# Optimization experiments

Hardware: AMD Instinct MI355X
Metric: run time of the kernel (lower is better)

Reference implementation:

```python
import jax, jax.numpy as jnp
import numpy as np

B, T, D, H, L = 16384, 100, 5, 32, 1  # batch, seq_len, input/output dim, hidden, latent


def setup_inputs() -> dict:
    key = jax.random.key(0)
    ks = jax.random.split(key, 28)
    rn = lambda k, shp, s=0.1: jax.random.normal(k, shp, dtype=jnp.float32) * s
    return {
        "x": rn(ks[0], (B, T, D), 1.0),
        "eps": rn(ks[1], (B, L), 1.0),
        # Encoder LSTM (PyTorch layout: W_ih [4H, D], W_hh [4H, H], gate order i,f,g,o)
        "enc_Wih": rn(ks[2], (4 * H, D)), "enc_Whh": rn(ks[3], (4 * H, H)),
        "enc_bih": rn(ks[4], (4 * H,)), "enc_bhh": rn(ks[5], (4 * H,)),
        "W_mu": rn(ks[6], (L, 2 * H)), "b_mu": rn(ks[7], (L,)),
        "W_lv": rn(ks[8], (L, 2 * H)), "b_lv": rn(ks[9], (L,)),
        # Decoder
        "W_l2h": rn(ks[10], (H, L)), "b_l2h": rn(ks[11], (H,)),
        "W_l2h2": rn(ks[12], (H, L)), "b_l2h2": rn(ks[13], (H,)),
        "start_token": jnp.zeros((1, D), jnp.float32),
        "W_emb": rn(ks[14], (H, D)), "b_emb": rn(ks[15], (H,)),
        "dec_Wih": rn(ks[16], (4 * H, H)), "dec_Whh": rn(ks[17], (4 * H, H)),
        "dec_bih": rn(ks[18], (4 * H,)), "dec_bhh": rn(ks[19], (4 * H,)),
        "W_out": rn(ks[20], (D, H)), "b_out": rn(ks[21], (D,)),
        "W_seq": rn(ks[22], (H, L)), "b_seq": rn(ks[23], (H,)),
        "W_seq2": rn(ks[24], (1, H)), "b_seq2": rn(ks[25], (1,)),
    }


def _lstm_cell(x_t, h, c, Wih, Whh, b):
    g = x_t @ Wih.T + h @ Whh.T + b            # [B, 4H]
    i, f, gg, o = jnp.split(g, 4, axis=-1)      # PyTorch gate order i,f,g,o
    c = jax.nn.sigmoid(f) * c + jax.nn.sigmoid(i) * jnp.tanh(gg)
    h = jax.nn.sigmoid(o) * jnp.tanh(c)
    return h, c


def reference(x, eps, enc_Wih, enc_Whh, enc_bih, enc_bhh, W_mu, b_mu, W_lv, b_lv,
              W_l2h, b_l2h, W_l2h2, b_l2h2, start_token, W_emb, b_emb,
              dec_Wih, dec_Whh, dec_bih, dec_bhh, W_out, b_out,
              W_seq, b_seq, W_seq2, b_seq2):
    bsz, seq_len, _ = x.shape
    hdim = enc_Whh.shape[1]
    lrelu = lambda v: jax.nn.leaky_relu(v, negative_slope=0.01)

    # ---- Encoder LSTM over time ----
    b_enc = enc_bih + enc_bhh
    def enc_step(carry, x_t):
        h, c = carry
        h, c = _lstm_cell(x_t, h, c, enc_Wih, enc_Whh, b_enc)
        return (h, c), None
    z0 = jnp.zeros((bsz, hdim), x.dtype)
    (h_n, c_n), _ = jax.lax.scan(enc_step, (z0, z0), jnp.swapaxes(x, 0, 1))
    hcat = jnp.concatenate([h_n, c_n], axis=-1)        # [B, 2H]
    mu = hcat @ W_mu.T + b_mu                           # [B, L]
    log_var = hcat @ W_lv.T + b_lv                      # [B, L]

    # ---- Reparameterize ----
    z = mu + eps * jnp.exp(0.5 * log_var)

    h0 = lrelu(mu @ W_l2h.T + b_l2h)                    # [B, H]
    c0 = lrelu(mu @ W_l2h2.T + b_l2h2)                  # [B, H]
    x0 = jnp.broadcast_to(start_token @ W_emb.T + b_emb, (bsz, hdim))
    b_dec = dec_bih + dec_bhh
    def dec_step(carry, _):
        x_in, h, c = carry
        x_t = jax.nn.relu(x_in)
        h, c = _lstm_cell(x_t, h, c, dec_Wih, dec_Whh, b_dec)
        return (h, h, c), h
    _, hs = jax.lax.scan(dec_step, (x0, h0, c0), None, length=seq_len)  # [T, B, H]
    recon = jnp.swapaxes(hs, 0, 1) @ W_out.T + b_out    # [B, T, D]

    # ---- num head on z (encoder_outputs arg) ----
    num = jax.nn.relu(lrelu(z @ W_seq.T + b_seq) @ W_seq2.T + b_seq2)  # [B, 1]

    return recon, mu, log_var, num
```

## Files before the change

### kernel.cpp

```cpp
#include <hip/hip_runtime.h>
#include <hip/hip_bf16.h>

typedef short bf16x8 __attribute__((ext_vector_type(8)));
typedef float f32x4  __attribute__((ext_vector_type(4)));
typedef unsigned int u32x4 __attribute__((ext_vector_type(4)));

#define LOG2E 1.44269504088896340736f

static __device__ __forceinline__ unsigned short f2bf(float f){
    __hip_bfloat16 h = __float2bfloat16(f);
    return __builtin_bit_cast(unsigned short, h);
}
static __device__ __forceinline__ float bf2f(unsigned short u){
    unsigned v = ((unsigned)u) << 16;
    return __builtin_bit_cast(float, v);
}
static __device__ __forceinline__ unsigned pk_bf16(float lo, float hi){
    return (((unsigned)f2bf(hi)) << 16) | (unsigned)f2bf(lo);
}
static __device__ __forceinline__ float rcp_(float x){ return __builtin_amdgcn_rcpf(x); }
static __device__ __forceinline__ float ex2(float x){ return __builtin_amdgcn_exp2f(x); }
static __device__ __forceinline__ void lds_fence(){
    asm volatile("s_waitcnt lgkmcnt(0)" ::: "memory");
}
static __device__ __forceinline__ f32x4 mfma16(bf16x8 a, bf16x8 b, f32x4 c){
    return __builtin_amdgcn_mfma_f32_16x16x32_bf16(a, b, c, 0, 0, 0);
}

__global__ void marker_kernel(float* out, int n, float v){
    int i = blockIdx.x * 256 + threadIdx.x;
    if (i < n) out[i] = v;
}

__global__ __launch_bounds__(256, 1)
void vae_mfma3_kernel(const float* __restrict__ x,      const float* __restrict__ eps,
                      const float* __restrict__ eWih,   const float* __restrict__ eWhh,
                      const float* __restrict__ ebih,   const float* __restrict__ ebhh,
                      const float* __restrict__ Wmu,    const float* __restrict__ bmu,
                      const float* __restrict__ Wlv,    const float* __restrict__ blv,
                      const float* __restrict__ Wl2h,   const float* __restrict__ bl2h,
                      const float* __restrict__ Wl2h2,  const float* __restrict__ bl2h2,
                      const float* __restrict__ stok,   const float* __restrict__ Wemb,
                      const float* __restrict__ bemb,
                      const float* __restrict__ dWih,   const float* __restrict__ dWhh,
                      const float* __restrict__ dbih,   const float* __restrict__ dbhh,
                      const float* __restrict__ Wout,   const float* __restrict__ bout,
                      const float* __restrict__ Wseq,   const float* __restrict__ bseq,
                      const float* __restrict__ Wseq2,  const float* __restrict__ bseq2,
                      float* __restrict__ recon,
                      float* __restrict__ out_mu,
                      float* __restrict__ out_lv,
                      float* __restrict__ out_num)
{
    __shared__ float hbf[4][16][33];
    __shared__ float cbf[4][16][33];
    __shared__ float mubuf[4][16];
    __shared__ float x0buf[4][32];
    __shared__ float cw[524];

    const int tid = threadIdx.x;
    const int w   = tid >> 6;
    const int l   = tid & 63;
    const int c   = l & 15;
    const int g   = l >> 4;
    const int bbase = blockIdx.x * 64 + w * 16;

    if (tid < 64){ cw[tid] = Wmu[tid]; cw[64+tid] = Wlv[tid]; }
    if (tid < 32){
        cw[128+tid] = Wseq[tid];  cw[160+tid] = bseq[tid];  cw[192+tid] = Wseq2[tid];
        cw[224+tid] = Wl2h[tid];  cw[256+tid] = bl2h[tid];
        cw[288+tid] = Wl2h2[tid]; cw[320+tid] = bl2h2[tid];
    }
    if (tid < 160) cw[352+tid] = Wout[tid];
    if (tid < 5)   cw[512+tid] = bout[tid];
    if (tid == 0){ cw[517] = bmu[0]; cw[518] = blv[0]; cw[519] = bseq2[0]; }
    __syncthreads();

    bf16x8 WH[8], WX[8];
    f32x4  biasv[8];
    #pragma unroll
    for (int n=0;n<8;++n){
        const int gt = n>>1, half = n&1;
        const float sc = (gt==2) ? (-2.0f*LOG2E) : (-LOG2E);
        const int GRc = gt*32 + ((c>>2)<<3) + half*4 + (c&3);
        bf16x8 t;
        #pragma unroll
        for (int j=0;j<8;++j) t[j] = (short)f2bf(sc * eWhh[(size_t)GRc*32 + g*8 + j]);
        WH[n] = t;
        bf16x8 tx = (bf16x8)0;
        if (g == 0){
            #pragma unroll
            for (int j=0;j<5;++j) tx[j] = (short)f2bf(sc * eWih[(size_t)GRc*5 + j]);
        }
        WX[n] = tx;
        f32x4 b4;
        #pragma unroll
        for (int q=0;q<4;++q){
            const int R = gt*32 + g*8 + half*4 + q;
            b4[q] = sc * (ebih[R] + ebhh[R]);
        }
        biasv[n] = b4;
    }

    float cs[8], hn[8];
    #pragma unroll
    for (int k=0;k<8;++k){ cs[k] = 0.0f; hn[k] = 0.0f; }
    u32x4 hpk = (u32x4)0;

    float4 xA = {0,0,0,0}; float xB = 0.0f;
    if (g == 0){
        const float* xp = x + (size_t)(bbase+c)*500;
        xA = *(const float4*)xp; xB = xp[4];
    }

    for (int t=0; t<100; ++t){
        bf16x8 bx = (bf16x8)0;
        if (g == 0){
            bx[0]=(short)f2bf(xA.x); bx[1]=(short)f2bf(xA.y);
            bx[2]=(short)f2bf(xA.z); bx[3]=(short)f2bf(xA.w);
            bx[4]=(short)f2bf(xB);
            if (t < 99){
                const float* xp = x + (size_t)(bbase+c)*500 + (t+1)*5;
                xA = *(const float4*)xp; xB = xp[4];
            }
        }
        bf16x8 bh = __builtin_bit_cast(bf16x8, hpk);

        f32x4 acc[8];
        #pragma unroll
        for (int n=0;n<8;++n){
            f32x4 a = mfma16(WX[n], bx, biasv[n]);
            acc[n] = mfma16(WH[n], bh, a);
        }

        #pragma unroll
        for (int q=0;q<4;++q){
          #pragma unroll
          for (int u=0;u<2;++u){
            const int ul = u*4 + q;
            float ei = ex2(acc[0+u][q]);
            float ef = ex2(acc[2+u][q]);
            float eg = ex2(acc[4+u][q]);
            float eo = ex2(acc[6+u][q]);
            float pig = (1.0f+ei)*(1.0f+eg);
            float num = cs[ul]*pig + (1.0f+ef)*(1.0f-eg);
            float cn  = num * rcp_((1.0f+ef)*pig);
            float ec  = ex2(cn * (-2.0f*LOG2E));
            hn[ul]    = (1.0f-ec) * rcp_((1.0f+eo)*(1.0f+ec));
            cs[ul]    = cn;
          }
        }
        hpk[0] = pk_bf16(hn[0], hn[1]);
        hpk[1] = pk_bf16(hn[2], hn[3]);
        hpk[2] = pk_bf16(hn[4], hn[5]);
        hpk[3] = pk_bf16(hn[6], hn[7]);
    }

    #pragma unroll
    for (int ul=0; ul<8; ++ul){
        hbf[w][c][g*8+ul] = hn[ul];
        cbf[w][c][g*8+ul] = cs[ul];
    }
    lds_fence();

    bf16x8 WI[8], WHd[8];
    f32x4  dbias[8];
    #pragma unroll
    for (int n=0;n<8;++n){
        const int gt = n>>1, half = n&1;
        const float sc = (gt==2) ? (-2.0f*LOG2E) : (-LOG2E);
        const int GRc = gt*32 + ((c>>2)<<3) + half*4 + (c&3);
        bf16x8 ti, th;
        #pragma unroll
        for (int j=0;j<8;++j){
            ti[j] = (short)f2bf(sc * dWih[(size_t)GRc*32 + g*8 + j]);
            th[j] = (short)f2bf(sc * dWhh[(size_t)GRc*32 + g*8 + j]);
        }
        WI[n] = ti; WHd[n] = th;
        f32x4 b4;
        #pragma unroll
        for (int q=0;q<4;++q){
            const int R = gt*32 + g*8 + half*4 + q;
            b4[q] = sc * (dbih[R] + dbhh[R]);
        }
        dbias[n] = b4;
    }
    bf16x8 WO = (bf16x8)0;
    f32x4 bosv = (f32x4)0;
    if (c < 5){
        bf16x8 to;
        #pragma unroll
        for (int j=0;j<8;++j) to[j] = (short)f2bf(Wout[c*32 + g*8 + j]);
        WO = to;
    }
    #pragma unroll
    for (int q=0;q<4;++q){
        const int dd = g*4 + q;
        bosv[q] = (dd < 5) ? bout[dd] : 0.0f;
    }

    if (l < 16){
        const int r = l;
        float mu = cw[517], lv = cw[518];
        #pragma unroll
        for (int k=0;k<32;++k){
            float hvv = hbf[w][r][k], cvv = cbf[w][r][k];
            mu += hvv*cw[k]    + cvv*cw[32+k];
            lv += hvv*cw[64+k] + cvv*cw[96+k];
        }
        out_mu[bbase+r] = mu;
        out_lv[bbase+r] = lv;
        mubuf[w][r] = mu;
        float z = mu + eps[bbase+r] * __builtin_amdgcn_exp2f(0.5f*LOG2E*lv);
        float a2 = cw[519];
        #pragma unroll
        for (int j=0;j<32;++j){
            float s = z*cw[128+j] + cw[160+j];
            s = s > 0.0f ? s : 0.01f*s;
            a2 += cw[192+j]*s;
        }
        out_num[bbase+r] = fmaxf(a2, 0.0f);
    }
    if (l < 32){
        float v = bemb[l];
        #pragma unroll
        for (int d=0; d<5; ++d) v += stok[d]*Wemb[l*5 + d];
        x0buf[w][l] = fmaxf(v, 0.0f);
    }
    lds_fence();

    {
        const float muv = mubuf[w][c];
        #pragma unroll
        for (int ul=0; ul<8; ++ul){
            const int U = g*8 + ul;
            float a = muv*cw[224+U] + cw[256+U];
            float b = muv*cw[288+U] + cw[320+U];
            hn[ul] = (a > 0.0f ? a : 0.01f*a);
            cs[ul] = (b > 0.0f ? b : 0.01f*b);
        }
        hpk[0] = pk_bf16(hn[0], hn[1]);
        hpk[1] = pk_bf16(hn[2], hn[3]);
        hpk[2] = pk_bf16(hn[4], hn[5]);
        hpk[3] = pk_bf16(hn[6], hn[7]);
    }
    bf16x8 bx0;
    #pragma unroll
    for (int j=0;j<8;++j) bx0[j] = (short)f2bf(x0buf[w][g*8 + j]);

    for (int t=0; t<100; ++t){
        bf16x8 bh = __builtin_bit_cast(bf16x8, hpk);

        if (t > 0){
            f32x4 ao = mfma16(WO, bh, bosv);
            float* rp = recon + (size_t)(bbase+c)*500 + (t-1)*5;
            if (g == 0){ rp[0]=ao[0]; rp[1]=ao[1]; rp[2]=ao[2]; rp[3]=ao[3]; }
            else if (g == 1){ rp[4]=ao[0]; }
        }

        bf16x8 bx;
        if (t == 0) bx = bx0;
        else {
            u32x4 rv;
            #pragma unroll
            for (int i=0;i<4;++i){
                unsigned v = hpk[i];
                unsigned m = ((v >> 15) & 0x00010001u) * 0xFFFFu;
                rv[i] = v & ~m;
            }
            bx = __builtin_bit_cast(bf16x8, rv);
        }

        f32x4 acc[8];
        #pragma unroll
        for (int n=0;n<8;++n){
            f32x4 a = mfma16(WI[n], bx, dbias[n]);
            acc[n] = mfma16(WHd[n], bh, a);
        }

        #pragma unroll
        for (int q=0;q<4;++q){
          #pragma unroll
          for (int u=0;u<2;++u){
            const int ul = u*4 + q;
            float ei = ex2(acc[0+u][q]);
            float ef = ex2(acc[2+u][q]);
            float eg = ex2(acc[4+u][q]);
            float eo = ex2(acc[6+u][q]);
            float pig = (1.0f+ei)*(1.0f+eg);
            float num = cs[ul]*pig + (1.0f+ef)*(1.0f-eg);
            float cn  = num * rcp_((1.0f+ef)*pig);
            float ec  = ex2(cn * (-2.0f*LOG2E));
            hn[ul]    = (1.0f-ec) * rcp_((1.0f+eo)*(1.0f+ec));
            cs[ul]    = cn;
          }
        }
        hpk[0] = pk_bf16(hn[0], hn[1]);
        hpk[1] = pk_bf16(hn[2], hn[3]);
        hpk[2] = pk_bf16(hn[4], hn[5]);
        hpk[3] = pk_bf16(hn[6], hn[7]);
    }

    {
        bf16x8 bh = __builtin_bit_cast(bf16x8, hpk);
        f32x4 ao = mfma16(WO, bh, bosv);
        float* rp = recon + (size_t)(bbase+c)*500 + 99*5;
        if (g == 0){ rp[0]=ao[0]; rp[1]=ao[1]; rp[2]=ao[2]; rp[3]=ao[3]; }
        else if (g == 1){ rp[4]=ao[0]; }
    }
}

extern "C" void kernel_launch(void* const* d_in, const int* in_sizes, int n_in,
                              void* d_out, int out_size, void* d_ws, size_t ws_size,
                              hipStream_t stream)
{
    (void)d_ws; (void)ws_size;
    static const int EXPECT[27] = {8192000,16384,640,4096,128,128,64,1,64,1,
                                   32,32,32,32,5,160,32,4096,4096,128,128,
                                   160,5,32,32,32,1};
    bool in_ok = (n_in == 27);
    if (in_ok) for (int i = 0; i < 27; ++i) in_ok = in_ok && (in_sizes[i] == EXPECT[i]);
    bool out_ok = (out_size == 8241152);

    float* out = (float*)d_out;
    if (!in_ok){
        marker_kernel<<<(out_size + 255)/256, 256, 0, stream>>>(out, out_size, 2.0f);
        return;
    }
    if (!out_ok){
        marker_kernel<<<(out_size + 255)/256, 256, 0, stream>>>(out, out_size, 3.0f);
        return;
    }

    const float* x     = (const float*)d_in[0];
    const float* eps   = (const float*)d_in[1];
    const float* eWih  = (const float*)d_in[2];
    const float* eWhh  = (const float*)d_in[3];
    const float* ebih  = (const float*)d_in[4];
    const float* ebhh  = (const float*)d_in[5];
    const float* Wmu   = (const float*)d_in[6];
    const float* bmu   = (const float*)d_in[7];
    const float* Wlv   = (const float*)d_in[8];
    const float* blv   = (const float*)d_in[9];
    const float* Wl2h  = (const float*)d_in[10];
    const float* bl2h  = (const float*)d_in[11];
    const float* Wl2h2 = (const float*)d_in[12];
    const float* bl2h2 = (const float*)d_in[13];
    const float* stok  = (const float*)d_in[14];
    const float* Wemb  = (const float*)d_in[15];
    const float* bemb  = (const float*)d_in[16];
    const float* dWih  = (const float*)d_in[17];
    const float* dWhh  = (const float*)d_in[18];
    const float* dbih  = (const float*)d_in[19];
    const float* dbhh  = (const float*)d_in[20];
    const float* Wout  = (const float*)d_in[21];
    const float* bout  = (const float*)d_in[22];
    const float* Wseq  = (const float*)d_in[23];
    const float* bseq  = (const float*)d_in[24];
    const float* Wseq2 = (const float*)d_in[25];
    const float* bseq2 = (const float*)d_in[26];

    float* recon  = out;
    float* out_mu = out + 8192000;
    float* out_lv = out_mu + 16384;
    float* out_nm = out_lv + 16384;

    vae_mfma3_kernel<<<256, 256, 0, stream>>>(x, eps,
        eWih, eWhh, ebih, ebhh, Wmu, bmu, Wlv, blv,
        Wl2h, bl2h, Wl2h2, bl2h2, stok, Wemb, bemb,
        dWih, dWhh, dbih, dbhh, Wout, bout,
        Wseq, bseq, Wseq2, bseq2,
        recon, out_mu, out_lv, out_nm);
}
```

Before: 136.9 us.

## Halve batch per wave, split hidden units across lane halves with swizzle exchange

Each wave now processes 8 batch rows instead of 16. The two halves of the 16-column MFMA tile compute different hidden-unit halves of the same rows, so each lane evaluates 4 gate activations instead of 8. The halves exchange packed h values through ds_swizzle, and the grid doubles to 512 blocks with launch bounds raised to 2 blocks per CU. This halves the per-lane transcendental work on the serial recurrence critical path and doubles the parallelism across the 256 CUs. In exchange, the MFMA count per batch row doubles and a cross-lane swizzle is added every step.

```diff
diff --git a/kernel.cpp b/kernel.cpp
--- a/kernel.cpp
+++ b/kernel.cpp
@@ -10,10 +10,6 @@
 static __device__ __forceinline__ unsigned short f2bf(float f){
     __hip_bfloat16 h = __float2bfloat16(f);
     return __builtin_bit_cast(unsigned short, h);
-}
-static __device__ __forceinline__ float bf2f(unsigned short u){
-    unsigned v = ((unsigned)u) << 16;
-    return __builtin_bit_cast(float, v);
 }
 static __device__ __forceinline__ unsigned pk_bf16(float lo, float hi){
     return (((unsigned)f2bf(hi)) << 16) | (unsigned)f2bf(lo);
@@ -26,14 +22,17 @@
 static __device__ __forceinline__ f32x4 mfma16(bf16x8 a, bf16x8 b, f32x4 c){
     return __builtin_amdgcn_mfma_f32_16x16x32_bf16(a, b, c, 0, 0, 0);
 }
+static __device__ __forceinline__ unsigned swz8(unsigned v){
+    return (unsigned)__builtin_amdgcn_ds_swizzle((int)v, 0x201F);
+}
 
 __global__ void marker_kernel(float* out, int n, float v){
     int i = blockIdx.x * 256 + threadIdx.x;
     if (i < n) out[i] = v;
 }
 
-__global__ __launch_bounds__(256, 1)
-void vae_mfma3_kernel(const float* __restrict__ x,      const float* __restrict__ eps,
+__global__ __launch_bounds__(256, 2)
+void vae_mfma4_kernel(const float* __restrict__ x,      const float* __restrict__ eps,
                       const float* __restrict__ eWih,   const float* __restrict__ eWhh,
                       const float* __restrict__ ebih,   const float* __restrict__ ebhh,
                       const float* __restrict__ Wmu,    const float* __restrict__ bmu,
@@ -52,9 +51,9 @@
                       float* __restrict__ out_lv,
                       float* __restrict__ out_num)
 {
-    __shared__ float hbf[4][16][33];
-    __shared__ float cbf[4][16][33];
-    __shared__ float mubuf[4][16];
+    __shared__ float hbf[4][8][33];
+    __shared__ float cbf[4][8][33];
+    __shared__ float mubuf[4][8];
     __shared__ float x0buf[4][32];
     __shared__ float cw[524];
 
@@ -63,7 +62,9 @@
     const int l   = tid & 63;
     const int c   = l & 15;
     const int g   = l >> 4;
-    const int bbase = blockIdx.x * 64 + w * 16;
+    const int ch  = c >> 3;
+    const int bb  = c & 7;
+    const int bbase = blockIdx.x * 32 + w * 8;
 
     if (tid < 64){ cw[tid] = Wmu[tid]; cw[64+tid] = Wlv[tid]; }
     if (tid < 32){
@@ -102,14 +103,14 @@
         biasv[n] = b4;
     }
 
-    float cs[8], hn[8];
-    #pragma unroll
-    for (int k=0;k<8;++k){ cs[k] = 0.0f; hn[k] = 0.0f; }
+    float cs[4], hn[4];
+    #pragma unroll
+    for (int k=0;k<4;++k){ cs[k] = 0.0f; hn[k] = 0.0f; }
     u32x4 hpk = (u32x4)0;
 
     float4 xA = {0,0,0,0}; float xB = 0.0f;
     if (g == 0){
-        const float* xp = x + (size_t)(bbase+c)*500;
+        const float* xp = x + (size_t)(bbase+bb)*500;
         xA = *(const float4*)xp; xB = xp[4];
     }
 
@@ -120,7 +121,7 @@
             bx[2]=(short)f2bf(xA.z); bx[3]=(short)f2bf(xA.w);
             bx[4]=(short)f2bf(xB);
             if (t < 99){
-                const float* xp = x + (size_t)(bbase+c)*500 + (t+1)*5;
+                const float* xp = x + (size_t)(bbase+bb)*500 + (t+1)*5;
                 xA = *(const float4*)xp; xB = xp[4];
             }
         }
@@ -133,33 +134,39 @@
             acc[n] = mfma16(WH[n], bh, a);
         }
 
-        #pragma unroll
-        for (int q=0;q<4;++q){
-          #pragma unroll
-          for (int u=0;u<2;++u){
-            const int ul = u*4 + q;
-            float ei = ex2(acc[0+u][q]);
-            float ef = ex2(acc[2+u][q]);
-            float eg = ex2(acc[4+u][q]);
-            float eo = ex2(acc[6+u][q]);
+        f32x4 ai = ch ? acc[1] : acc[0];
+        f32x4 af = ch ? acc[3] : acc[2];
+        f32x4 ag = ch ? acc[5] : acc[4];
+        f32x4 ao = ch ? acc[7] : acc[6];
+
+        #pragma unroll
+        for (int q=0;q<4;++q){
+            float ei = ex2(ai[q]);
+            float ef = ex2(af[q]);
+            float eg = ex2(ag[q]);
+            float eo = ex2(ao[q]);
             float pig = (1.0f+ei)*(1.0f+eg);
-            float num = cs[ul]*pig + (1.0f+ef)*(1.0f-eg);
+            float num = cs[q]*pig + (1.0f+ef)*(1.0f-eg);
             float cn  = num * rcp_((1.0f+ef)*pig);
             float ec  = ex2(cn * (-2.0f*LOG2E));
-            hn[ul]    = (1.0f-ec) * rcp_((1.0f+eo)*(1.0f+ec));
-            cs[ul]    = cn;
-          }
-        }
-        hpk[0] = pk_bf16(hn[0], hn[1]);
-        hpk[1] = pk_bf16(hn[2], hn[3]);
-        hpk[2] = pk_bf16(hn[4], hn[5]);
-        hpk[3] = pk_bf16(hn[6], hn[7]);
-    }
-
-    #pragma unroll
-    for (int ul=0; ul<8; ++ul){
-        hbf[w][c][g*8+ul] = hn[ul];
-        cbf[w][c][g*8+ul] = cs[ul];
+            hn[q]     = (1.0f-ec) * rcp_((1.0f+eo)*(1.0f+ec));
+            cs[q]     = cn;
+        }
+        unsigned wA = pk_bf16(hn[0], hn[1]);
+        unsigned wB = pk_bf16(hn[2], hn[3]);
+        unsigned rA = swz8(wA);
+        unsigned rB = swz8(wB);
+        hpk[0] = ch ? rA : wA;
+        hpk[1] = ch ? rB : wB;
+        hpk[2] = ch ? wA : rA;
+        hpk[3] = ch ? wB : rB;
+    }
+
+    #pragma unroll
+    for (int q=0;q<4;++q){
+        const int U = g*8 + ch*4 + q;
+        hbf[w][bb][U] = hn[q];
+        cbf[w][bb][U] = cs[q];
     }
     lds_fence();
 
@@ -199,7 +206,7 @@
         bosv[q] = (dd < 5) ? bout[dd] : 0.0f;
     }
 
-    if (l < 16){
+    if (l < 8){
         const int r = l;
         float mu = cw[517], lv = cw[518];
         #pragma unroll
@@ -230,19 +237,24 @@
     lds_fence();
 
     {
-        const float muv = mubuf[w][c];
+        const float muv = mubuf[w][bb];
+        float h8[8];
         #pragma unroll
         for (int ul=0; ul<8; ++ul){
             const int U = g*8 + ul;
             float a = muv*cw[224+U] + cw[256+U];
+            h8[ul] = (a > 0.0f ? a : 0.01f*a);
+        }
+        #pragma unroll
+        for (int q=0;q<4;++q){
+            const int U = g*8 + ch*4 + q;
             float b = muv*cw[288+U] + cw[320+U];
-            hn[ul] = (a > 0.0f ? a : 0.01f*a);
-            cs[ul] = (b > 0.0f ? b : 0.01f*b);
-        }
-        hpk[0] = pk_bf16(hn[0], hn[1]);
-        hpk[1] = pk_bf16(hn[2], hn[3]);
-        hpk[2] = pk_bf16(hn[4], hn[5]);
-        hpk[3] = pk_bf16(hn[6], hn[7]);
+            cs[q] = (b > 0.0f ? b : 0.01f*b);
+        }
+        hpk[0] = pk_bf16(h8[0], h8[1]);
+        hpk[1] = pk_bf16(h8[2], h8[3]);
+        hpk[2] = pk_bf16(h8[4], h8[5]);
+        hpk[3] = pk_bf16(h8[6], h8[7]);
     }
     bf16x8 bx0;
     #pragma unroll
@@ -252,10 +264,12 @@
         bf16x8 bh = __builtin_bit_cast(bf16x8, hpk);
 
         if (t > 0){
-            f32x4 ao = mfma16(WO, bh, bosv);
-            float* rp = recon + (size_t)(bbase+c)*500 + (t-1)*5;
-            if (g == 0){ rp[0]=ao[0]; rp[1]=ao[1]; rp[2]=ao[2]; rp[3]=ao[3]; }
-            else if (g == 1){ rp[4]=ao[0]; }
+            f32x4 aoo = mfma16(WO, bh, bosv);
+            if (c < 8){
+                float* rp = recon + (size_t)(bbase+bb)*500 + (t-1)*5;
+                if (g == 0){ rp[0]=aoo[0]; rp[1]=aoo[1]; rp[2]=aoo[2]; rp[3]=aoo[3]; }
+                else if (g == 1){ rp[4]=aoo[0]; }
+            }
         }
 
         bf16x8 bx;
@@ -278,35 +292,42 @@
             acc[n] = mfma16(WHd[n], bh, a);
         }
 
-        #pragma unroll
-        for (int q=0;q<4;++q){
-          #pragma unroll
-          for (int u=0;u<2;++u){
-            const int ul = u*4 + q;
-            float ei = ex2(acc[0+u][q]);
-            float ef = ex2(acc[2+u][q]);
-            float eg = ex2(acc[4+u][q]);
-            float eo = ex2(acc[6+u][q]);
+        f32x4 ai = ch ? acc[1] : acc[0];
+        f32x4 af = ch ? acc[3] : acc[2];
+        f32x4 ag = ch ? acc[5] : acc[4];
+        f32x4 ao = ch ? acc[7] : acc[6];
+
+        #pragma unroll
+        for (int q=0;q<4;++q){
+            float ei = ex2(ai[q]);
+            float ef = ex2(af[q]);
+            float eg = ex2(ag[q]);
+            float eo = ex2(ao[q]);
             float pig = (1.0f+ei)*(1.0f+eg);
-            float num = cs[ul]*pig + (1.0f+ef)*(1.0f-eg);
+            float num = cs[q]*pig + (1.0f+ef)*(1.0f-eg);
             float cn  = num * rcp_((1.0f+ef)*pig);
             float ec  = ex2(cn * (-2.0f*LOG2E));
-            hn[ul]    = (1.0f-ec) * rcp_((1.0f+eo)*(1.0f+ec));
-            cs[ul]    = cn;
-          }
-        }
-        hpk[0] = pk_bf16(hn[0], hn[1]);
-        hpk[1] = pk_bf16(hn[2], hn[3]);
-        hpk[2] = pk_bf16(hn[4], hn[5]);
-        hpk[3] = pk_bf16(hn[6], hn[7]);
+            hn[q]     = (1.0f-ec) * rcp_((1.0f+eo)*(1.0f+ec));
+            cs[q]     = cn;
+        }
+        unsigned wA = pk_bf16(hn[0], hn[1]);
+        unsigned wB = pk_bf16(hn[2], hn[3]);
+        unsigned rA = swz8(wA);
+        unsigned rB = swz8(wB);
+        hpk[0] = ch ? rA : wA;
+        hpk[1] = ch ? rB : wB;
+        hpk[2] = ch ? wA : rA;
+        hpk[3] = ch ? wB : rB;
     }
 
     {
         bf16x8 bh = __builtin_bit_cast(bf16x8, hpk);
-        f32x4 ao = mfma16(WO, bh, bosv);
-        float* rp = recon + (size_t)(bbase+c)*500 + 99*5;
-        if (g == 0){ rp[0]=ao[0]; rp[1]=ao[1]; rp[2]=ao[2]; rp[3]=ao[3]; }
-        else if (g == 1){ rp[4]=ao[0]; }
+        f32x4 aoo = mfma16(WO, bh, bosv);
+        if (c < 8){
+            float* rp = recon + (size_t)(bbase+bb)*500 + 99*5;
+            if (g == 0){ rp[0]=aoo[0]; rp[1]=aoo[1]; rp[2]=aoo[2]; rp[3]=aoo[3]; }
+            else if (g == 1){ rp[4]=aoo[0]; }
+        }
     }
 }
 
@@ -365,7 +386,7 @@
     float* out_lv = out_mu + 16384;
     float* out_nm = out_lv + 16384;
 
-    vae_mfma3_kernel<<<256, 256, 0, stream>>>(x, eps,
+    vae_mfma4_kernel<<<512, 256, 0, stream>>>(x, eps,
         eWih, eWhh, ebih, ebhh, Wmu, bmu, Wlv, blv,
         Wl2h, bl2h, Wl2h2, bl2h2, stok, Wemb, bemb,
         dWih, dWhh, dbih, dbhh, Wout, bout,
```

After: 175.8 us. 1.28x slower.

## Split LSTM hidden units across two waves exchanging h via LDS double buffer

Applied to the files above, without the earlier changes.

Each 16-row batch tile is now handled by a pair of waves, each computing half of the hidden units (4 MFMA gate tiles instead of 8), with the new h exchanged through a double-buffered LDS array and a block barrier every timestep. The grid doubles to 512 blocks of 32 rows, and launch bounds allow two blocks per CU. The aim is to halve the serial per-step work per wave and raise occupancy to hide MFMA and transcendental latency. The cost is an LDS round trip plus __syncthreads on every one of the 200 recurrent steps.

```diff
diff --git a/kernel.cpp b/kernel.cpp
--- a/kernel.cpp
+++ b/kernel.cpp
@@ -11,20 +11,17 @@
     __hip_bfloat16 h = __float2bfloat16(f);
     return __builtin_bit_cast(unsigned short, h);
 }
-static __device__ __forceinline__ float bf2f(unsigned short u){
-    unsigned v = ((unsigned)u) << 16;
-    return __builtin_bit_cast(float, v);
-}
 static __device__ __forceinline__ unsigned pk_bf16(float lo, float hi){
     return (((unsigned)f2bf(hi)) << 16) | (unsigned)f2bf(lo);
 }
 static __device__ __forceinline__ float rcp_(float x){ return __builtin_amdgcn_rcpf(x); }
 static __device__ __forceinline__ float ex2(float x){ return __builtin_amdgcn_exp2f(x); }
-static __device__ __forceinline__ void lds_fence(){
-    asm volatile("s_waitcnt lgkmcnt(0)" ::: "memory");
-}
 static __device__ __forceinline__ f32x4 mfma16(bf16x8 a, bf16x8 b, f32x4 c){
     return __builtin_amdgcn_mfma_f32_16x16x32_bf16(a, b, c, 0, 0, 0);
+}
+static __device__ __forceinline__ unsigned relu_pk(unsigned v){
+    unsigned m = ((v >> 15) & 0x00010001u) * 0xFFFFu;
+    return v & ~m;
 }
 
 __global__ void marker_kernel(float* out, int n, float v){
@@ -32,8 +29,8 @@
     if (i < n) out[i] = v;
 }
 
-__global__ __launch_bounds__(256, 1)
-void vae_mfma3_kernel(const float* __restrict__ x,      const float* __restrict__ eps,
+__global__ __launch_bounds__(256, 2)
+void vae_mfma6_kernel(const float* __restrict__ x,      const float* __restrict__ eps,
                       const float* __restrict__ eWih,   const float* __restrict__ eWhh,
                       const float* __restrict__ ebih,   const float* __restrict__ ebhh,
                       const float* __restrict__ Wmu,    const float* __restrict__ bmu,
@@ -52,18 +49,21 @@
                       float* __restrict__ out_lv,
                       float* __restrict__ out_num)
 {
-    __shared__ float hbf[4][16][33];
-    __shared__ float cbf[4][16][33];
-    __shared__ float mubuf[4][16];
-    __shared__ float x0buf[4][32];
+    __shared__ unsigned hx[2][2][16][20];
+    __shared__ float hbf[2][16][33];
+    __shared__ float cbf[2][16][33];
+    __shared__ float mubuf[2][16];
+    __shared__ float x0buf[32];
     __shared__ float cw[524];
 
     const int tid = threadIdx.x;
     const int w   = tid >> 6;
+    const int W   = w & 1;
+    const int pi  = w >> 1;
     const int l   = tid & 63;
     const int c   = l & 15;
     const int g   = l >> 4;
-    const int bbase = blockIdx.x * 64 + w * 16;
+    const int bbase = blockIdx.x * 32 + pi * 16;
 
     if (tid < 64){ cw[tid] = Wmu[tid]; cw[64+tid] = Wlv[tid]; }
     if (tid < 32){
@@ -74,38 +74,39 @@
     if (tid < 160) cw[352+tid] = Wout[tid];
     if (tid < 5)   cw[512+tid] = bout[tid];
     if (tid == 0){ cw[517] = bmu[0]; cw[518] = blv[0]; cw[519] = bseq2[0]; }
-    __syncthreads();
-
-    bf16x8 WH[8], WX[8];
-    f32x4  biasv[8];
-    #pragma unroll
-    for (int n=0;n<8;++n){
-        const int gt = n>>1, half = n&1;
-        const float sc = (gt==2) ? (-2.0f*LOG2E) : (-LOG2E);
-        const int GRc = gt*32 + ((c>>2)<<3) + half*4 + (c&3);
+
+    bf16x8 WH[4], WX[4];
+    f32x4  biasv[4];
+    #pragma unroll
+    for (int n=0;n<4;++n){
+        const float sc = (n==2) ? (-2.0f*LOG2E) : (-LOG2E);
+        const int GR = n*32 + W*16 + c;
         bf16x8 t;
         #pragma unroll
-        for (int j=0;j<8;++j) t[j] = (short)f2bf(sc * eWhh[(size_t)GRc*32 + g*8 + j]);
+        for (int j=0;j<8;++j) t[j] = (short)f2bf(sc * eWhh[(size_t)GR*32 + g*8 + j]);
         WH[n] = t;
         bf16x8 tx = (bf16x8)0;
         if (g == 0){
             #pragma unroll
-            for (int j=0;j<5;++j) tx[j] = (short)f2bf(sc * eWih[(size_t)GRc*5 + j]);
+            for (int j=0;j<5;++j) tx[j] = (short)f2bf(sc * eWih[(size_t)GR*5 + j]);
         }
         WX[n] = tx;
         f32x4 b4;
         #pragma unroll
         for (int q=0;q<4;++q){
-            const int R = gt*32 + g*8 + half*4 + q;
+            const int R = n*32 + W*16 + g*4 + q;
             b4[q] = sc * (ebih[R] + ebhh[R]);
         }
         biasv[n] = b4;
     }
 
-    float cs[8], hn[8];
-    #pragma unroll
-    for (int k=0;k<8;++k){ cs[k] = 0.0f; hn[k] = 0.0f; }
-    u32x4 hpk = (u32x4)0;
+    float cs[4], hn[4];
+    #pragma unroll
+    for (int k=0;k<4;++k){ cs[k] = 0.0f; hn[k] = 0.0f; }
+
+    *(uint2*)&hx[0][pi][c][W*8 + g*2] = make_uint2(0u, 0u);
+    int p = 0;
+    __syncthreads();
 
     float4 xA = {0,0,0,0}; float xB = 0.0f;
     if (g == 0){
@@ -114,6 +115,9 @@
     }
 
     for (int t=0; t<100; ++t){
+        u32x4 hw = *(const u32x4*)&hx[p][pi][c][g*4];
+        bf16x8 bh = __builtin_bit_cast(bf16x8, hw);
+
         bf16x8 bx = (bf16x8)0;
         if (g == 0){
             bx[0]=(short)f2bf(xA.x); bx[1]=(short)f2bf(xA.y);
@@ -124,63 +128,57 @@
                 xA = *(const float4*)xp; xB = xp[4];
             }
         }
-        bf16x8 bh = __builtin_bit_cast(bf16x8, hpk);
-
-        f32x4 acc[8];
-        #pragma unroll
-        for (int n=0;n<8;++n){
-            f32x4 a = mfma16(WX[n], bx, biasv[n]);
-            acc[n] = mfma16(WH[n], bh, a);
-        }
-
-        #pragma unroll
-        for (int q=0;q<4;++q){
-          #pragma unroll
-          for (int u=0;u<2;++u){
-            const int ul = u*4 + q;
-            float ei = ex2(acc[0+u][q]);
-            float ef = ex2(acc[2+u][q]);
-            float eg = ex2(acc[4+u][q]);
-            float eo = ex2(acc[6+u][q]);
+
+        f32x4 acc[4];
+        #pragma unroll
+        for (int n=0;n<4;++n) acc[n] = mfma16(WX[n], bx, biasv[n]);
+        #pragma unroll
+        for (int n=0;n<4;++n) acc[n] = mfma16(WH[n], bh, acc[n]);
+
+        #pragma unroll
+        for (int q=0;q<4;++q){
+            float ei = ex2(acc[0][q]);
+            float ef = ex2(acc[1][q]);
+            float eg = ex2(acc[2][q]);
+            float eo = ex2(acc[3][q]);
             float pig = (1.0f+ei)*(1.0f+eg);
-            float num = cs[ul]*pig + (1.0f+ef)*(1.0f-eg);
+            float num = cs[q]*pig + (1.0f+ef)*(1.0f-eg);
             float cn  = num * rcp_((1.0f+ef)*pig);
             float ec  = ex2(cn * (-2.0f*LOG2E));
-            hn[ul]    = (1.0f-ec) * rcp_((1.0f+eo)*(1.0f+ec));
-            cs[ul]    = cn;
-          }
-        }
-        hpk[0] = pk_bf16(hn[0], hn[1]);
-        hpk[1] = pk_bf16(hn[2], hn[3]);
-        hpk[2] = pk_bf16(hn[4], hn[5]);
-        hpk[3] = pk_bf16(hn[6], hn[7]);
-    }
-
-    #pragma unroll
-    for (int ul=0; ul<8; ++ul){
-        hbf[w][c][g*8+ul] = hn[ul];
-        cbf[w][c][g*8+ul] = cs[ul];
-    }
-    lds_fence();
-
-    bf16x8 WI[8], WHd[8];
-    f32x4  dbias[8];
-    #pragma unroll
-    for (int n=0;n<8;++n){
-        const int gt = n>>1, half = n&1;
-        const float sc = (gt==2) ? (-2.0f*LOG2E) : (-LOG2E);
-        const int GRc = gt*32 + ((c>>2)<<3) + half*4 + (c&3);
+            hn[q]     = (1.0f-ec) * rcp_((1.0f+eo)*(1.0f+ec));
+            cs[q]     = cn;
+        }
+        *(uint2*)&hx[p^1][pi][c][W*8 + g*2] =
+            make_uint2(pk_bf16(hn[0], hn[1]), pk_bf16(hn[2], hn[3]));
+        __syncthreads();
+        p ^= 1;
+    }
+
+    #pragma unroll
+    for (int q=0;q<4;++q){
+        const int U = W*16 + g*4 + q;
+        hbf[pi][c][U] = hn[q];
+        cbf[pi][c][U] = cs[q];
+    }
+    __syncthreads();
+
+    bf16x8 WI[4], WHd[4];
+    f32x4  dbias[4];
+    #pragma unroll
+    for (int n=0;n<4;++n){
+        const float sc = (n==2) ? (-2.0f*LOG2E) : (-LOG2E);
+        const int GR = n*32 + W*16 + c;
         bf16x8 ti, th;
         #pragma unroll
         for (int j=0;j<8;++j){
-            ti[j] = (short)f2bf(sc * dWih[(size_t)GRc*32 + g*8 + j]);
-            th[j] = (short)f2bf(sc * dWhh[(size_t)GRc*32 + g*8 + j]);
+            ti[j] = (short)f2bf(sc * dWih[(size_t)GR*32 + g*8 + j]);
+            th[j] = (short)f2bf(sc * dWhh[(size_t)GR*32 + g*8 + j]);
         }
         WI[n] = ti; WHd[n] = th;
         f32x4 b4;
         #pragma unroll
         for (int q=0;q<4;++q){
-            const int R = gt*32 + g*8 + half*4 + q;
+            const int R = n*32 + W*16 + g*4 + q;
             b4[q] = sc * (dbih[R] + dbhh[R]);
         }
         dbias[n] = b4;
@@ -199,19 +197,20 @@
         bosv[q] = (dd < 5) ? bout[dd] : 0.0f;
     }
 
-    if (l < 16){
-        const int r = l;
+    if (tid < 32){
+        const int pr = tid >> 4, rr = tid & 15;
+        const int row = blockIdx.x*32 + tid;
         float mu = cw[517], lv = cw[518];
         #pragma unroll
         for (int k=0;k<32;++k){
-            float hvv = hbf[w][r][k], cvv = cbf[w][r][k];
+            float hvv = hbf[pr][rr][k], cvv = cbf[pr][rr][k];
             mu += hvv*cw[k]    + cvv*cw[32+k];
             lv += hvv*cw[64+k] + cvv*cw[96+k];
         }
-        out_mu[bbase+r] = mu;
-        out_lv[bbase+r] = lv;
-        mubuf[w][r] = mu;
-        float z = mu + eps[bbase+r] * __builtin_amdgcn_exp2f(0.5f*LOG2E*lv);
+        out_mu[row] = mu;
+        out_lv[row] = lv;
+        mubuf[pr][rr] = mu;
+        float z = mu + eps[row] * __builtin_amdgcn_exp2f(0.5f*LOG2E*lv);
         float a2 = cw[519];
         #pragma unroll
         for (int j=0;j<32;++j){
@@ -219,91 +218,83 @@
             s = s > 0.0f ? s : 0.01f*s;
             a2 += cw[192+j]*s;
         }
-        out_num[bbase+r] = fmaxf(a2, 0.0f);
-    }
-    if (l < 32){
-        float v = bemb[l];
-        #pragma unroll
-        for (int d=0; d<5; ++d) v += stok[d]*Wemb[l*5 + d];
-        x0buf[w][l] = fmaxf(v, 0.0f);
-    }
-    lds_fence();
+        out_num[row] = fmaxf(a2, 0.0f);
+        float v = bemb[tid];
+        #pragma unroll
+        for (int d=0; d<5; ++d) v += stok[d]*Wemb[tid*5 + d];
+        x0buf[tid] = fmaxf(v, 0.0f);
+    }
+    __syncthreads();
 
     {
-        const float muv = mubuf[w][c];
-        #pragma unroll
-        for (int ul=0; ul<8; ++ul){
-            const int U = g*8 + ul;
+        const float muv = mubuf[pi][c];
+        float h4[4];
+        #pragma unroll
+        for (int q=0;q<4;++q){
+            const int U = W*16 + g*4 + q;
             float a = muv*cw[224+U] + cw[256+U];
             float b = muv*cw[288+U] + cw[320+U];
-            hn[ul] = (a > 0.0f ? a : 0.01f*a);
-            cs[ul] = (b > 0.0f ? b : 0.01f*b);
-        }
-        hpk[0] = pk_bf16(hn[0], hn[1]);
-        hpk[1] = pk_bf16(hn[2], hn[3]);
-        hpk[2] = pk_bf16(hn[4], hn[5]);
-        hpk[3] = pk_bf16(hn[6], hn[7]);
-    }
+            h4[q]  = (a > 0.0f ? a : 0.01f*a);
+            cs[q]  = (b > 0.0f ? b : 0.01f*b);
+        }
+        *(uint2*)&hx[0][pi][c][W*8 + g*2] =
+            make_uint2(pk_bf16(h4[0], h4[1]), pk_bf16(h4[2], h4[3]));
+    }
+    p = 0;
+    __syncthreads();
+
     bf16x8 bx0;
     #pragma unroll
-    for (int j=0;j<8;++j) bx0[j] = (short)f2bf(x0buf[w][g*8 + j]);
+    for (int j=0;j<8;++j) bx0[j] = (short)f2bf(x0buf[g*8 + j]);
 
     for (int t=0; t<100; ++t){
-        bf16x8 bh = __builtin_bit_cast(bf16x8, hpk);
-
-        if (t > 0){
-            f32x4 ao = mfma16(WO, bh, bosv);
-            float* rp = recon + (size_t)(bbase+c)*500 + (t-1)*5;
-            if (g == 0){ rp[0]=ao[0]; rp[1]=ao[1]; rp[2]=ao[2]; rp[3]=ao[3]; }
-            else if (g == 1){ rp[4]=ao[0]; }
-        }
+        u32x4 hw = *(const u32x4*)&hx[p][pi][c][g*4];
+        bf16x8 bh = __builtin_bit_cast(bf16x8, hw);
 
         bf16x8 bx;
         if (t == 0) bx = bx0;
         else {
             u32x4 rv;
             #pragma unroll
-            for (int i=0;i<4;++i){
-                unsigned v = hpk[i];
-                unsigned m = ((v >> 15) & 0x00010001u) * 0xFFFFu;
-                rv[i] = v & ~m;
-            }
+            for (int i=0;i<4;++i) rv[i] = relu_pk(hw[i]);
             bx = __builtin_bit_cast(bf16x8, rv);
         }
 
-        f32x4 acc[8];
-        #pragma unroll
-        for (int n=0;n<8;++n){
-            f32x4 a = mfma16(WI[n], bx, dbias[n]);
-            acc[n] = mfma16(WHd[n], bh, a);
-        }
-
-        #pragma unroll
-        for (int q=0;q<4;++q){
-          #pragma unroll
-          for (int u=0;u<2;++u){
-            const int ul = u*4 + q;
-            float ei = ex2(acc[0+u][q]);
-            float ef = ex2(acc[2+u][q]);
-            float eg = ex2(acc[4+u][q]);
-            float eo = ex2(acc[6+u][q]);
+        f32x4 acc[4];
+        #pragma unroll
+        for (int n=0;n<4;++n) acc[n] = mfma16(WI[n], bx, dbias[n]);
+        #pragma unroll
+        for (int n=0;n<4;++n) acc[n] = mfma16(WHd[n], bh, acc[n]);
+
+        if (W == 0 && t > 0){
+            f32x4 ao = mfma16(WO, bh, bosv);
+            float* rp = recon + (size_t)(bbase+c)*500 + (t-1)*5;
+            if (g == 0){ rp[0]=ao[0]; rp[1]=ao[1]; rp[2]=ao[2]; rp[3]=ao[3]; }
+            else if (g == 1){ rp[4]=ao[0]; }
+        }
+
+        #pragma unroll
+        for (int q=0;q<4;++q){
+            float ei = ex2(acc[0][q]);
+            float ef = ex2(acc[1][q]);
+            float eg = ex2(acc[2][q]);
+            float eo = ex2(acc[3][q]);
             float pig = (1.0f+ei)*(1.0f+eg);
-            float num = cs[ul]*pig + (1.0f+ef)*(1.0f-eg);
+            float num = cs[q]*pig + (1.0f+ef)*(1.0f-eg);
             float cn  = num * rcp_((1.0f+ef)*pig);
             float ec  = ex2(cn * (-2.0f*LOG2E));
-            hn[ul]    = (1.0f-ec) * rcp_((1.0f+eo)*(1.0f+ec));
-            cs[ul]    = cn;
-          }
-        }
-        hpk[0] = pk_bf16(hn[0], hn[1]);
-        hpk[1] = pk_bf16(hn[2], hn[3]);
-        hpk[2] = pk_bf16(hn[4], hn[5]);
-        hpk[3] = pk_bf16(hn[6], hn[7]);
-    }
-
-    {
-        bf16x8 bh = __builtin_bit_cast(bf16x8, hpk);
-        f32x4 ao = mfma16(WO, bh, bosv);
+            hn[q]     = (1.0f-ec) * rcp_((1.0f+eo)*(1.0f+ec));
+            cs[q]     = cn;
+        }
+        *(uint2*)&hx[p^1][pi][c][W*8 + g*2] =
+            make_uint2(pk_bf16(hn[0], hn[1]), pk_bf16(hn[2], hn[3]));
+        __syncthreads();
+        p ^= 1;
+    }
+
+    if (W == 0){
+        u32x4 hw = *(const u32x4*)&hx[p][pi][c][g*4];
+        f32x4 ao = mfma16(WO, __builtin_bit_cast(bf16x8, hw), bosv);
         float* rp = recon + (size_t)(bbase+c)*500 + 99*5;
         if (g == 0){ rp[0]=ao[0]; rp[1]=ao[1]; rp[2]=ao[2]; rp[3]=ao[3]; }
         else if (g == 1){ rp[4]=ao[0]; }
@@ -365,7 +356,7 @@
     float* out_lv = out_mu + 16384;
     float* out_nm = out_lv + 16384;
 
-    vae_mfma3_kernel<<<256, 256, 0, stream>>>(x, eps,
+    vae_mfma6_kernel<<<512, 256, 0, stream>>>(x, eps,
         eWih, eWhh, ebih, ebhh, Wmu, bmu, Wlv, blv,
         Wl2h, bl2h, Wl2h2, bl2h2, stok, Wemb, bemb,
         dWih, dWhh, dbih, dbhh, Wout, bout,
```

New measurement: 142.9 us. +4.3%, slower.
